# Performance work log

Measured on AMD Instinct MI355X. Metric: run time of the kernel, lower is better.

## Reference

```python
import jax, jax.numpy as jnp
import numpy as np

B, S, E = 2, 2048, 1024          # batch, seq, emb_size
H, D = 16, 64                     # heads, head_dim
NE, K = 8, 2                      # num_experts, top_k


def setup_inputs() -> dict:
    key = jax.random.key(0)
    ks = jax.random.split(key, 12)
    w = lambda k, shape: jax.random.normal(k, shape, jnp.float32) * 0.02
    return {
        "x": jax.random.normal(ks[0], (B, S, E), jnp.float32),
        "q_w": w(ks[1], (E, E)), "q_b": jnp.zeros((E,), jnp.float32),
        "k_w": w(ks[2], (E, E)), "k_b": jnp.zeros((E,), jnp.float32),
        "v_w": w(ks[3], (E, E)), "v_b": jnp.zeros((E,), jnp.float32),
        "gate_w": w(ks[4], (NE, E)), "gate_b": jnp.zeros((NE,), jnp.float32),
        "expert_w": w(ks[5], (NE, E, E)), "expert_b": jnp.zeros((NE, E), jnp.float32),
        "ffn_w": w(ks[6], (E, E)), "ffn_b": jnp.zeros((E,), jnp.float32),
    }


def _rope_cos_sin(seq_len, dim):
    inv_freq = 1.0 / (10000.0 ** (jnp.arange(0, dim, 2, dtype=jnp.float32) / dim))
    freqs = jnp.outer(jnp.arange(seq_len, dtype=jnp.float32), inv_freq)  # [S, D/2]
    emb = jnp.concatenate([freqs, freqs], axis=-1)                        # [S, D]
    return jnp.cos(emb), jnp.sin(emb)


def _rotate_half(x):
    x1, x2 = jnp.split(x, 2, axis=-1)
    return jnp.concatenate([-x2, x1], axis=-1)


def reference(x, q_w, q_b, k_w, k_b, v_w, v_b, gate_w, gate_b, expert_w, expert_b, ffn_w, ffn_b):
    b, s, _ = x.shape
    q = (x @ q_w.T + q_b).reshape(b, s, H, D)
    k = (x @ k_w.T + k_b).reshape(b, s, H, D)
    v = (x @ v_w.T + v_b).reshape(b, s, H, D)

    cos, sin = _rope_cos_sin(s, D)          # [S, D]
    cos = cos[None, :, None, :]
    sin = sin[None, :, None, :]
    q = q * cos + _rotate_half(q) * sin
    k = k * cos + _rotate_half(k) * sin

    # full (memory-efficient-style) attention, scale 1/sqrt(D)
    scores = jnp.einsum('bqhd,bkhd->bhqk', q, k) / jnp.sqrt(jnp.float32(D))
    attn = jax.nn.softmax(scores, axis=-1)
    attn_out = jnp.einsum('bhqk,bkhd->bqhd', attn, v).reshape(b, s, E)

    # MoE: dense-compute all experts, gather top-k, weighted combine
    gates = jax.nn.softmax(attn_out @ gate_w.T + gate_b, axis=-1)        # [B,S,NE]
    top_gates, top_idx = jax.lax.top_k(gates, K)                          # [B,S,K]
    # Linear per expert: y = x W^T + b,  expert_w: [NE, out, in]
    expert_outputs = jnp.einsum('bsi,noi->bsno', attn_out, expert_w) + expert_b  # [B,S,NE,E]
    sel = jnp.take_along_axis(expert_outputs, top_idx[..., None], axis=2)        # [B,S,K,E]
    moe_out = jnp.einsum('bsk,bskh->bsh', top_gates, sel)                        # [B,S,E]

    # dropout is identity at inference; ffn + residual
    return moe_out @ ffn_w.T + ffn_b + x
```

## Files before the change

### kernel.cpp

```cpp
#include <hip/hip_runtime.h>
#include <hip/hip_bf16.h>

#define B_ 2
#define S_ 2048
#define E_ 1024
#define H_ 16
#define D_ 64
#define NE_ 8
#define TOKENS (B_*S_)
#define QSCALE 0.18033688011112043f

typedef __attribute__((ext_vector_type(8))) short bf16x8;
typedef __attribute__((ext_vector_type(4))) float f32x4;
typedef __attribute__((ext_vector_type(16))) float f32x16;
typedef unsigned short u16;
typedef unsigned int u32;
typedef __attribute__((ext_vector_type(4))) u32 u32x4;

#if __has_builtin(__builtin_amdgcn_exp2f)
#define EXP2(x) __builtin_amdgcn_exp2f(x)
#else
#define EXP2(x) exp2f(x)
#endif

__device__ __forceinline__ u16 f2bf(float f) {
    u32 u = __float_as_uint(f);
    u32 r = u + 0x7fffu + ((u >> 16) & 1u);
    return (u16)(r >> 16);
}
__device__ __forceinline__ float bf2f(u16 h) {
    return __uint_as_float(((u32)h) << 16);
}
__device__ __forceinline__ void gl2lds16(const void* g, void* l) {
    __builtin_amdgcn_global_load_lds(
        (__attribute__((address_space(1))) void*)(g),
        (__attribute__((address_space(3))) void*)(l), 16, 0, 0);
}
#define MFMA16(a,b,c) __builtin_amdgcn_mfma_f32_16x16x32_bf16(a,b,c,0,0,0)
#define MFMA32(a,b,c) __builtin_amdgcn_mfma_f32_32x32x16_bf16(a,b,c,0,0,0)

__global__ void cvt_all_k(
    const float* __restrict__ x,  const float* __restrict__ qw,
    const float* __restrict__ kw, const float* __restrict__ vw,
    const float* __restrict__ fw, const float* __restrict__ ew,
    u16* __restrict__ xh,  u16* __restrict__ qwh, u16* __restrict__ kwh,
    u16* __restrict__ vwh, u16* __restrict__ fwh, u16* __restrict__ ewh,
    float2* __restrict__ tab)
{
    const int blk = blockIdx.x;
    if (blk >= 16384) {
        const int idx = (blk - 16384) * 256 + threadIdx.x;
        const int s = idx >> 5, d1 = idx & 31;
        const float inv = exp2f(-(float)d1 * 0.41524101186091903f);
        float sn, cs;
        sincosf((float)s * inv, &sn, &cs);
        tab[idx] = make_float2(cs, sn);
        return;
    }
    const float* s; u16* d; int off;
    if (blk < 4096)      { s = x;  d = xh;  off = blk; }
    else if (blk < 5120) { s = qw; d = qwh; off = blk - 4096; }
    else if (blk < 6144) { s = kw; d = kwh; off = blk - 5120; }
    else if (blk < 7168) { s = vw; d = vwh; off = blk - 6144; }
    else if (blk < 8192) { s = fw; d = fwh; off = blk - 7168; }
    else                 { s = ew; d = ewh; off = blk - 8192; }
    const size_t i = (size_t)off * 256 + threadIdx.x;
    const float4 v = *(const float4*)(s + i * 4);
    ushort4 H = {f2bf(v.x), f2bf(v.y), f2bf(v.z), f2bf(v.w)};
    *(ushort4*)(d + i * 4) = H;
}

__global__ __launch_bounds__(256,2) void gemm_qkv(
    const u16* __restrict__ Ah,
    const u16* __restrict__ qwh, const u16* __restrict__ kwh,
    const u16* __restrict__ vwh,
    const float* __restrict__ q_b, const float* __restrict__ k_b,
    const float* __restrict__ v_b,
    const float2* __restrict__ tab,
    u16* __restrict__ Qhb, u16* __restrict__ Khb, u16* __restrict__ Vtb)
{
    __shared__ __align__(16) u16 sA[128*32], sB[128*32];
    const int z = blockIdx.z;
    const u16* Bh = (z == 0) ? qwh : (z == 1) ? kwh : vwh;
    const float* bias = (z == 0) ? q_b : (z == 1) ? k_b : v_b;
    const int t = threadIdx.x;
    const int m0 = blockIdx.y * 128, n0 = blockIdx.x * 128;
    const int lane = t & 63, w = t >> 6;
    const int wm = w >> 1, wn = w & 1;
    const int lr = lane & 15, qd = lane >> 4;
    f32x4 acc[4][4] = {};
    const size_t gA = (size_t)(m0 + (t >> 2)) * E_ + (t & 3) * 8;
    const size_t gB = (size_t)(n0 + (t >> 2)) * E_ + (t & 3) * 8;
    for (int k0 = 0; k0 < E_; k0 += 32) {
        #pragma unroll
        for (int is = 0; is < 2; is++) {
            const int ldo = (is * 256 + (t & 192)) * 16;
            const size_t ro = (size_t)is * 64 * E_;
            gl2lds16(Ah + gA + ro + k0, (char*)sA + ldo);
            gl2lds16(Bh + gB + ro + k0, (char*)sB + ldo);
        }
        __syncthreads();
        bf16x8 af[4], bfr[4];
        #pragma unroll
        for (int i = 0; i < 4; i++) {
            af[i]  = *(const bf16x8*)&sA[(wm*64 + i*16 + lr)*32 + qd*8];
            bfr[i] = *(const bf16x8*)&sB[(wn*64 + i*16 + lr)*32 + qd*8];
        }
        #pragma unroll
        for (int i = 0; i < 4; i++)
            #pragma unroll
            for (int j = 0; j < 4; j++)
                acc[i][j] = MFMA16(af[i], bfr[j], acc[i][j]);
        __syncthreads();
    }
    const int head = (n0 + wn * 64) >> 6;
    if (z < 2) {
        u16* Oh = (z == 0) ? Qhb : Khb;
        const float osc = (z == 0) ? QSCALE : 1.0f;
        #pragma unroll
        for (int j = 0; j < 2; j++) {
            const int d1 = j * 16 + lr;
            const float b1 = bias[head * 64 + d1];
            const float b2 = bias[head * 64 + d1 + 32];
            #pragma unroll
            for (int i = 0; i < 4; i++) {
                #pragma unroll
                for (int r = 0; r < 4; r++) {
                    const int tok = m0 + wm*64 + i*16 + qd*4 + r;
                    const int bb = tok >> 11, ss = tok & (S_ - 1);
                    const float2 t2 = tab[ss * 32 + d1];
                    const float q1 = acc[i][j][r]   + b1;
                    const float q2 = acc[i][j+2][r] + b2;
                    const size_t o = (((size_t)bb * H_ + head) * S_ + ss) * 64 + d1;
                    Oh[o]    = f2bf((q1 * t2.x - q2 * t2.y) * osc);
                    Oh[o+32] = f2bf((q2 * t2.x + q1 * t2.y) * osc);
                }
            }
        }
    } else {
        #pragma unroll
        for (int j = 0; j < 4; j++) {
            const int d = j * 16 + lr;
            const float bv = bias[head * 64 + d];
            #pragma unroll
            for (int i = 0; i < 4; i++)
                #pragma unroll
                for (int r = 0; r < 4; r++) {
                    const int tok = m0 + wm*64 + i*16 + qd*4 + r;
                    const int bb = tok >> 11, ss = tok & (S_ - 1);
                    Vtb[(((size_t)bb * H_ + head) * 64 + d) * S_ + ss] = f2bf(acc[i][j][r] + bv);
                }
        }
    }
}

__global__ __launch_bounds__(256,4) void attn_kernel(
    const u16* __restrict__ Q, const u16* __restrict__ K,
    const u16* __restrict__ Vt,
    float* __restrict__ Opart, float* __restrict__ lpart)
{
    __shared__ __align__(16) u16 sK[2][64*64];
    __shared__ __align__(16) u16 sV[2][64*64];
    const int t = threadIdx.x, lane = t & 63, w = t >> 6;
    const int lq = lane & 31, hi = lane >> 5;
    const int lin = blockIdx.x + (blockIdx.y << 4) + (blockIdx.z << 8);
    const int wg  = ((lin & 7) << 7) + (lin >> 3);
    const int q0 = (wg & 15) << 7;
    const int h  = (wg >> 4) & 15;
    const int zc = wg >> 8;
    const int b = zc & 1, sc = zc >> 1;
    const size_t bhS = ((size_t)b * H_ + h) * S_;
    const size_t bhD = ((size_t)b * H_ + h) * 64;
    bf16x8 qf[4];
    #pragma unroll
    for (int ks = 0; ks < 4; ks++)
        qf[ks] = *(const bf16x8*)&Q[(bhS + q0 + w*32 + lq) * 64 + ks*16 + hi*8];
    bf16x8 vOnes;
    #pragma unroll
    for (int i = 0; i < 8; i++) vOnes[i] = (short)0x3F80;
    f32x16 O[2] = {};
    f32x16 Ol = {};

    const int f0 = w*2, f1 = w*2 + 1;
    const int kR0 = (f0>>2)*32 + lq, kC0 = (f0&3)*16 + hi*8;
    const int kR1 = (f1>>2)*32 + lq, kC1 = (f1&3)*16 + hi*8;
    auto stage = [&](int bp, int j0) {
        gl2lds16(&K [(bhS + j0 + kR0)*64 + kC0], (char*)sK[bp] + f0*1024);
        gl2lds16(&K [(bhS + j0 + kR1)*64 + kC1], (char*)sK[bp] + f1*1024);
        gl2lds16(&Vt[(bhD + kR0)*S_ + j0 + kC0], (char*)sV[bp] + f0*1024);
        gl2lds16(&Vt[(bhD + kR1)*S_ + j0 + kC1], (char*)sV[bp] + f1*1024);
    };

    const int jbeg = sc * 1024;
    stage(0, jbeg);
    for (int jt = 0; jt < 16; ++jt) {
        const int cur = jt & 1;
        asm volatile("s_waitcnt vmcnt(0) lgkmcnt(0)" ::: "memory");
        __builtin_amdgcn_sched_barrier(0);
        __builtin_amdgcn_s_barrier();
        __builtin_amdgcn_sched_barrier(0);
        if (jt + 1 < 16) stage(cur ^ 1, jbeg + (jt + 1) * 64);
        u32 pk[16];
        #pragma unroll
        for (int kb = 0; kb < 2; kb++) {
            f32x16 Sv = {};
            __builtin_amdgcn_s_setprio(1);
            #pragma unroll
            for (int ks = 0; ks < 4; ks++) {
                const bf16x8 kf = *(const bf16x8*)&sK[cur][(kb*4 + ks)*512 + lane*8];
                Sv = MFMA32(kf, qf[ks], Sv);
            }
            __builtin_amdgcn_s_setprio(0);
            #pragma unroll
            for (int j = 0; j < 8; j++) {
                const float e0 = EXP2(Sv[2*j]);
                const float e1 = EXP2(Sv[2*j+1]);
                pk[kb*8 + j] = __builtin_amdgcn_perm(__float_as_uint(e1),
                                                     __float_as_uint(e0), 0x07060302u);
            }
        }
        #pragma unroll
        for (int ks = 0; ks < 4; ks++) {
            const int base = (ks >> 1)*8 + (ks & 1)*4;
            u32 a0 = pk[base],     b0 = pk[base + 2];
            u32 a1 = pk[base + 1], b1 = pk[base + 3];
            asm("v_permlane32_swap_b32 %0, %1" : "+v"(a0), "+v"(b0));
            asm("v_permlane32_swap_b32 %0, %1" : "+v"(a1), "+v"(b1));
            u32x4 fv; fv.x = a0; fv.y = a1; fv.z = b0; fv.w = b1;
            const bf16x8 pa = __builtin_bit_cast(bf16x8, fv);
            const bf16x8 vf0 = *(const bf16x8*)&sV[cur][(0*4 + ks)*512 + lane*8];
            const bf16x8 vf1 = *(const bf16x8*)&sV[cur][(1*4 + ks)*512 + lane*8];
            __builtin_amdgcn_s_setprio(1);
            O[0] = MFMA32(pa, vf0, O[0]);
            O[1] = MFMA32(pa, vf1, O[1]);
            Ol   = MFMA32(pa, vOnes, Ol);
            __builtin_amdgcn_s_setprio(0);
        }
    }
    float* Op = Opart + (size_t)sc * TOKENS * E_;
    float* lp = lpart + (size_t)sc * TOKENS * H_;
    if (lq == 0) {
        #pragma unroll
        for (int r = 0; r < 16; r++) {
            const int qr = (r & 3) + 8*(r >> 2) + 4*hi;
            lp[(size_t)(b*S_ + q0 + w*32 + qr) * H_ + h] = Ol[r];
        }
    }
    #pragma unroll
    for (int cb = 0; cb < 2; cb++)
        #pragma unroll
        for (int r = 0; r < 16; r++) {
            const int qr = (r & 3) + 8*(r >> 2) + 4*hi;
            Op[(size_t)(b*S_ + q0 + w*32 + qr) * E_ + h*64 + cb*32 + lq] = O[cb][r];
        }
}

__global__ __launch_bounds__(256) void combine_gate(
    const float* __restrict__ Opart, const float* __restrict__ lpart,
    const float* __restrict__ gate_w, const float* __restrict__ gate_b,
    u16* __restrict__ attn_bf, float* __restrict__ gval, int* __restrict__ eidx)
{
    __shared__ float red[4][NE_];
    __shared__ float lg8[NE_];
    const int tok = blockIdx.x;
    const int t = threadIdx.x;
    const int d4 = t * 4;
    const int h = d4 >> 6;
    const float l = lpart[(size_t)tok*H_ + h] + lpart[(size_t)(TOKENS + tok)*H_ + h];
    const float inv = 1.f / l;
    const float4 o1 = *(const float4*)&Opart[(size_t)tok*E_ + d4];
    const float4 o2 = *(const float4*)&Opart[(size_t)(TOKENS + tok)*E_ + d4];
    float v[4] = {(o1.x+o2.x)*inv, (o1.y+o2.y)*inv, (o1.z+o2.z)*inv, (o1.w+o2.w)*inv};
    ushort4 H4 = {f2bf(v[0]), f2bf(v[1]), f2bf(v[2]), f2bf(v[3])};
    *(ushort4*)&attn_bf[(size_t)tok*E_ + d4] = H4;
    float pe[NE_];
    #pragma unroll
    for (int e = 0; e < NE_; e++) {
        const float4 g = *(const float4*)&gate_w[e*E_ + d4];
        pe[e] = v[0]*g.x + v[1]*g.y + v[2]*g.z + v[3]*g.w;
    }
    #pragma unroll
    for (int e = 0; e < NE_; e++) {
        #pragma unroll
        for (int off = 32; off >= 1; off >>= 1)
            pe[e] += __shfl_xor(pe[e], off, 64);
    }
    const int w = t >> 6;
    if ((t & 63) == 0) {
        #pragma unroll
        for (int e = 0; e < NE_; e++) red[w][e] = pe[e];
    }
    __syncthreads();
    if (t < NE_)
        lg8[t] = red[0][t] + red[1][t] + red[2][t] + red[3][t] + gate_b[t];
    __syncthreads();
    if (t == 0) {
        float lg[NE_];
        #pragma unroll
        for (int e = 0; e < NE_; e++) lg[e] = lg8[e];
        float m = lg[0];
        #pragma unroll
        for (int e = 1; e < NE_; e++) m = fmaxf(m, lg[e]);
        float ex[NE_], ssum = 0.f;
        #pragma unroll
        for (int e = 0; e < NE_; e++) { ex[e] = __expf(lg[e]-m); ssum += ex[e]; }
        const float invs = 1.f / ssum;
        int i0 = 0;
        #pragma unroll
        for (int e = 1; e < NE_; e++) if (lg[e] > lg[i0]) i0 = e;
        int i1 = (i0 == 0) ? 1 : 0;
        #pragma unroll
        for (int e = 0; e < NE_; e++) if (e != i0 && lg[e] > lg[i1]) i1 = e;
        eidx[tok*2]     = i0;
        gval[tok*2]     = ex[i0]*invs;
        eidx[tok*2 + 1] = i1;
        gval[tok*2 + 1] = ex[i1]*invs;
    }
}

__global__ __launch_bounds__(256) void build_lists_kernel(
    const int* __restrict__ eidx, int* __restrict__ list, int* __restrict__ counts)
{
    __shared__ int lcnt[NE_], lbase[NE_];
    const int t = threadIdx.x;
    if (t < NE_) lcnt[t] = 0;
    __syncthreads();
    const int ent = blockIdx.x * 512 + t * 2;
    const int e0 = eidx[ent], e1 = eidx[ent + 1];
    const int p0 = atomicAdd(&lcnt[e0], 1);
    const int p1 = atomicAdd(&lcnt[e1], 1);
    __syncthreads();
    if (t < NE_) lbase[t] = atomicAdd(&counts[t], lcnt[t]);
    __syncthreads();
    list[e0 * TOKENS + lbase[e0] + p0] = ent;
    list[e1 * TOKENS + lbase[e1] + p1] = ent + 1;
}

__global__ __launch_bounds__(256,2) void gemm_expert(
    const u16* __restrict__ Abf, const u16* __restrict__ ewh,
    const float* __restrict__ eb, const int* __restrict__ list,
    const int* __restrict__ counts, const float* __restrict__ gval,
    u16* __restrict__ sel)
{
    const int e = blockIdx.z;
    const int cnt = counts[e];
    const int m0 = blockIdx.y * 128;
    if (m0 >= cnt) return;
    __shared__ __align__(16) u16 sA[128*32], sB[128*32];
    __shared__ int sEnt[128];
    const int t = threadIdx.x;
    if (t < 128) sEnt[t] = (m0 + t < cnt) ? list[e * TOKENS + m0 + t] : -1;
    __syncthreads();
    const int n0 = blockIdx.x * 128;
    const int lane = t & 63, w = t >> 6;
    const int wm = w >> 1, wn = w & 1;
    const int lr = lane & 15, qd = lane >> 4;
    const int e0 = sEnt[t >> 2], e1 = sEnt[64 + (t >> 2)];
    const u16* ga0 = Abf + (size_t)(e0 < 0 ? 0 : (e0 >> 1)) * E_ + (t & 3) * 8;
    const u16* ga1 = Abf + (size_t)(e1 < 0 ? 0 : (e1 >> 1)) * E_ + (t & 3) * 8;
    const u16* gb0 = ewh + (size_t)e * E_ * E_ + (size_t)(n0 + (t >> 2)) * E_ + (t & 3) * 8;
    const u16* gb1 = gb0 + 64 * E_;
    f32x4 acc[4][4] = {};
    for (int k0 = 0; k0 < E_; k0 += 32) {
        {
            const int l0 = (t & 192) * 16;
            const int l1 = (256 + (t & 192)) * 16;
            gl2lds16(ga0 + k0, (char*)sA + l0);
            gl2lds16(ga1 + k0, (char*)sA + l1);
            gl2lds16(gb0 + k0, (char*)sB + l0);
            gl2lds16(gb1 + k0, (char*)sB + l1);
        }
        __syncthreads();
        bf16x8 af[4], bfr[4];
        #pragma unroll
        for (int i = 0; i < 4; i++) {
            af[i]  = *(const bf16x8*)&sA[(wm*64 + i*16 + lr)*32 + qd*8];
            bfr[i] = *(const bf16x8*)&sB[(wn*64 + i*16 + lr)*32 + qd*8];
        }
        #pragma unroll
        for (int i = 0; i < 4; i++)
            #pragma unroll
            for (int j = 0; j < 4; j++)
                acc[i][j] = MFMA16(af[i], bfr[j], acc[i][j]);
        __syncthreads();
    }
    #pragma unroll
    for (int i = 0; i < 4; i++)
        #pragma unroll
        for (int r = 0; r < 4; r++) {
            const int local = wm*64 + i*16 + qd*4 + r;
            const int ent = sEnt[local];
            if (ent < 0) continue;
            const float g = gval[ent];
            #pragma unroll
            for (int j = 0; j < 4; j++) {
                const int col = n0 + wn*64 + j*16 + lr;
                sel[(size_t)ent * E_ + col] = f2bf((acc[i][j][r] + eb[e * E_ + col]) * g);
            }
        }
}

__global__ void combine_kernel(const u16* __restrict__ sel, u16* __restrict__ moe)
{
    const int g = blockIdx.x * 256 + threadIdx.x;
    const int tok = g >> 8;
    const int c = (g & 255) * 4;
    const u16* a = sel + (size_t)tok * 2048 + c;
    float o[4];
    #pragma unroll
    for (int j = 0; j < 4; j++) o[j] = bf2f(a[j]) + bf2f(a[1024 + j]);
    ushort4 R = {f2bf(o[0]), f2bf(o[1]), f2bf(o[2]), f2bf(o[3])};
    *(ushort4*)(moe + (size_t)tok * E_ + c) = R;
}

__global__ __launch_bounds__(256,2) void gemm_ffn(
    const u16* __restrict__ Ah, const u16* __restrict__ Bh,
    const float* __restrict__ bias, const float* __restrict__ res,
    float* __restrict__ C)
{
    __shared__ __align__(16) u16 sA[128*32], sB[128*32];
    const int t = threadIdx.x;
    const int m0 = blockIdx.y * 128, n0 = blockIdx.x * 128;
    const int lane = t & 63, w = t >> 6;
    const int wm = w >> 1, wn = w & 1;
    const int lr = lane & 15, qd = lane >> 4;
    f32x4 acc[4][4] = {};
    const size_t gA = (size_t)(m0 + (t >> 2)) * E_ + (t & 3) * 8;
    const size_t gB = (size_t)(n0 + (t >> 2)) * E_ + (t & 3) * 8;
    for (int k0 = 0; k0 < E_; k0 += 32) {
        #pragma unroll
        for (int is = 0; is < 2; is++) {
            const int ldo = (is * 256 + (t & 192)) * 16;
            const size_t ro = (size_t)is * 64 * E_;
            gl2lds16(Ah + gA + ro + k0, (char*)sA + ldo);
            gl2lds16(Bh + gB + ro + k0, (char*)sB + ldo);
        }
        __syncthreads();
        bf16x8 af[4], bfr[4];
        #pragma unroll
        for (int i = 0; i < 4; i++) {
            af[i]  = *(const bf16x8*)&sA[(wm*64 + i*16 + lr)*32 + qd*8];
            bfr[i] = *(const bf16x8*)&sB[(wn*64 + i*16 + lr)*32 + qd*8];
        }
        #pragma unroll
        for (int i = 0; i < 4; i++)
            #pragma unroll
            for (int j = 0; j < 4; j++)
                acc[i][j] = MFMA16(af[i], bfr[j], acc[i][j]);
        __syncthreads();
    }
    #pragma unroll
    for (int i = 0; i < 4; i++)
        #pragma unroll
        for (int r = 0; r < 4; r++) {
            const int tok = m0 + wm*64 + i*16 + qd*4 + r;
            #pragma unroll
            for (int j = 0; j < 4; j++) {
                const int col = n0 + wn*64 + j*16 + lr;
                C[(size_t)tok * E_ + col] = acc[i][j][r] + bias[col] + res[(size_t)tok * E_ + col];
            }
        }
}

extern "C" void kernel_launch(void* const* d_in, const int* in_sizes, int n_in,
                              void* d_out, int out_size, void* d_ws, size_t ws_size,
                              hipStream_t stream) {
    const float* x      = (const float*)d_in[0];
    const float* q_w    = (const float*)d_in[1];
    const float* q_b    = (const float*)d_in[2];
    const float* k_w    = (const float*)d_in[3];
    const float* k_b    = (const float*)d_in[4];
    const float* v_w    = (const float*)d_in[5];
    const float* v_b    = (const float*)d_in[6];
    const float* gate_w = (const float*)d_in[7];
    const float* gate_b = (const float*)d_in[8];
    const float* ew     = (const float*)d_in[9];
    const float* eb     = (const float*)d_in[10];
    const float* ffn_w  = (const float*)d_in[11];
    const float* ffn_b  = (const float*)d_in[12];
    float* out = (float*)d_out;

    char* p = (char*)d_ws;
    auto alloc = [&](size_t bytes) { char* r = p; p += (bytes + 255) & ~(size_t)255; return r; };
    u16* xh   = (u16*)alloc((size_t)TOKENS*E_*2);
    u16* qwh  = (u16*)alloc((size_t)E_*E_*2);
    u16* kwh  = (u16*)alloc((size_t)E_*E_*2);
    u16* vwh  = (u16*)alloc((size_t)E_*E_*2);
    u16* fwh  = (u16*)alloc((size_t)E_*E_*2);
    u16* ewh  = (u16*)alloc((size_t)NE_*E_*E_*2);
    u16* Qhb  = (u16*)alloc((size_t)TOKENS*E_*2);
    u16* Khb  = (u16*)alloc((size_t)TOKENS*E_*2);
    u16* Vtb  = (u16*)alloc((size_t)TOKENS*E_*2);
    u16* abf  = (u16*)alloc((size_t)TOKENS*E_*2);
    float* Opart = (float*)alloc((size_t)2*TOKENS*E_*4);
    float* lpart = (float*)alloc((size_t)2*TOKENS*H_*4);
    u16* selb = (u16*)alloc((size_t)2*TOKENS*E_*2);
    u16* moeb = (u16*)alloc((size_t)TOKENS*E_*2);
    float2* rtab = (float2*)alloc((size_t)S_*32*8);
    float* gvl = (float*)alloc((size_t)2*TOKENS*4);
    int*   eix = (int*)alloc((size_t)2*TOKENS*4);
    int*   lst = (int*)alloc((size_t)NE_*TOKENS*4);
    int*   cnt = (int*)alloc(256);

    hipMemsetAsync(cnt, 0, 256, stream);

    cvt_all_k<<<16640, 256, 0, stream>>>(x, q_w, k_w, v_w, ffn_w, ew,
                                         xh, qwh, kwh, vwh, fwh, ewh, rtab);

    gemm_qkv<<<dim3(8,32,3), 256, 0, stream>>>(xh, qwh, kwh, vwh,
                                               q_b, k_b, v_b, rtab,
                                               Qhb, Khb, Vtb);

    attn_kernel<<<dim3(16,16,4), 256, 0, stream>>>(Qhb, Khb, Vtb, Opart, lpart);

    combine_gate<<<TOKENS, 256, 0, stream>>>(Opart, lpart, gate_w, gate_b,
                                             abf, gvl, eix);
    build_lists_kernel<<<TOKENS/256, 256, 0, stream>>>(eix, lst, cnt);
    gemm_expert<<<dim3(8,32,8), 256, 0, stream>>>(abf, ewh, eb, lst, cnt, gvl, selb);
    combine_kernel<<<4096, 256, 0, stream>>>(selb, moeb);
    gemm_ffn<<<dim3(8,32), 256, 0, stream>>>(moeb, fwh, ffn_b, x, out);
}
```

Baseline: 297.9 us.

## Load K/V fragments directly from global into registers, dropping LDS staging

The attention kernel no longer stages K and V tiles through double-buffered shared memory with barriers. Each wave now loads its own K and V MFMA fragments straight from global memory into registers, and the loop is unrolled by two so loads can overlap compute. This removes LDS traffic and the per-tile block barrier. In exchange, the four waves of a block each fetch the same K/V data redundantly, register pressure rises (launch bounds lowered to 3 blocks per SM), and load latency is hidden only by unrolling and occupancy.

```diff
diff --git a/kernel.cpp b/kernel.cpp
--- a/kernel.cpp
+++ b/kernel.cpp
@@ -154,13 +154,11 @@
     }
 }
 
-__global__ __launch_bounds__(256,4) void attn_kernel(
+__global__ __launch_bounds__(256,3) void attn_kernel(
     const u16* __restrict__ Q, const u16* __restrict__ K,
     const u16* __restrict__ Vt,
     float* __restrict__ Opart, float* __restrict__ lpart)
 {
-    __shared__ __align__(16) u16 sK[2][64*64];
-    __shared__ __align__(16) u16 sV[2][64*64];
     const int t = threadIdx.x, lane = t & 63, w = t >> 6;
     const int lq = lane & 31, hi = lane >> 5;
     const int lin = blockIdx.x + (blockIdx.y << 4) + (blockIdx.z << 8);
@@ -178,45 +176,54 @@
     bf16x8 vOnes;
     #pragma unroll
     for (int i = 0; i < 8; i++) vOnes[i] = (short)0x3F80;
-    f32x16 O[2] = {};
+    f32x16 O0 = {}, O1 = {};
     f32x16 Ol = {};
 
-    const int f0 = w*2, f1 = w*2 + 1;
-    const int kR0 = (f0>>2)*32 + lq, kC0 = (f0&3)*16 + hi*8;
-    const int kR1 = (f1>>2)*32 + lq, kC1 = (f1&3)*16 + hi*8;
-    auto stage = [&](int bp, int j0) {
-        gl2lds16(&K [(bhS + j0 + kR0)*64 + kC0], (char*)sK[bp] + f0*1024);
-        gl2lds16(&K [(bhS + j0 + kR1)*64 + kC1], (char*)sK[bp] + f1*1024);
-        gl2lds16(&Vt[(bhD + kR0)*S_ + j0 + kC0], (char*)sV[bp] + f0*1024);
-        gl2lds16(&Vt[(bhD + kR1)*S_ + j0 + kC1], (char*)sV[bp] + f1*1024);
-    };
-
+    const u16* Kb = K  + (bhS + lq) * 64 + hi * 8;
+    const u16* Vb = Vt + (bhD + lq) * S_ + hi * 8;
     const int jbeg = sc * 1024;
-    stage(0, jbeg);
+
+    #pragma unroll 2
     for (int jt = 0; jt < 16; ++jt) {
-        const int cur = jt & 1;
-        asm volatile("s_waitcnt vmcnt(0) lgkmcnt(0)" ::: "memory");
-        __builtin_amdgcn_sched_barrier(0);
-        __builtin_amdgcn_s_barrier();
-        __builtin_amdgcn_sched_barrier(0);
-        if (jt + 1 < 16) stage(cur ^ 1, jbeg + (jt + 1) * 64);
+        const int j0 = jbeg + jt * 64;
+        bf16x8 kr0[4], kr1[4], vr0[4], vr1[4];
+        #pragma unroll
+        for (int ks = 0; ks < 4; ks++) {
+            kr0[ks] = *(const bf16x8*)(Kb + (size_t)j0 * 64 + ks*16);
+            kr1[ks] = *(const bf16x8*)(Kb + (size_t)(j0 + 32) * 64 + ks*16);
+        }
+        #pragma unroll
+        for (int ks = 0; ks < 4; ks++) {
+            vr0[ks] = *(const bf16x8*)(Vb + j0 + ks*16);
+            vr1[ks] = *(const bf16x8*)(Vb + (size_t)32 * S_ + j0 + ks*16);
+        }
         u32 pk[16];
-        #pragma unroll
-        for (int kb = 0; kb < 2; kb++) {
+        {
             f32x16 Sv = {};
             __builtin_amdgcn_s_setprio(1);
             #pragma unroll
-            for (int ks = 0; ks < 4; ks++) {
-                const bf16x8 kf = *(const bf16x8*)&sK[cur][(kb*4 + ks)*512 + lane*8];
-                Sv = MFMA32(kf, qf[ks], Sv);
-            }
+            for (int ks = 0; ks < 4; ks++) Sv = MFMA32(kr0[ks], qf[ks], Sv);
             __builtin_amdgcn_s_setprio(0);
             #pragma unroll
             for (int j = 0; j < 8; j++) {
                 const float e0 = EXP2(Sv[2*j]);
                 const float e1 = EXP2(Sv[2*j+1]);
-                pk[kb*8 + j] = __builtin_amdgcn_perm(__float_as_uint(e1),
-                                                     __float_as_uint(e0), 0x07060302u);
+                pk[j] = __builtin_amdgcn_perm(__float_as_uint(e1),
+                                              __float_as_uint(e0), 0x07060302u);
+            }
+        }
+        {
+            f32x16 Sv = {};
+            __builtin_amdgcn_s_setprio(1);
+            #pragma unroll
+            for (int ks = 0; ks < 4; ks++) Sv = MFMA32(kr1[ks], qf[ks], Sv);
+            __builtin_amdgcn_s_setprio(0);
+            #pragma unroll
+            for (int j = 0; j < 8; j++) {
+                const float e0 = EXP2(Sv[2*j]);
+                const float e1 = EXP2(Sv[2*j+1]);
+                pk[8 + j] = __builtin_amdgcn_perm(__float_as_uint(e1),
+                                                  __float_as_uint(e0), 0x07060302u);
             }
         }
         #pragma unroll
@@ -228,12 +235,10 @@
             asm("v_permlane32_swap_b32 %0, %1" : "+v"(a1), "+v"(b1));
             u32x4 fv; fv.x = a0; fv.y = a1; fv.z = b0; fv.w = b1;
             const bf16x8 pa = __builtin_bit_cast(bf16x8, fv);
-            const bf16x8 vf0 = *(const bf16x8*)&sV[cur][(0*4 + ks)*512 + lane*8];
-            const bf16x8 vf1 = *(const bf16x8*)&sV[cur][(1*4 + ks)*512 + lane*8];
             __builtin_amdgcn_s_setprio(1);
-            O[0] = MFMA32(pa, vf0, O[0]);
-            O[1] = MFMA32(pa, vf1, O[1]);
-            Ol   = MFMA32(pa, vOnes, Ol);
+            O0 = MFMA32(pa, vr0[ks], O0);
+            O1 = MFMA32(pa, vr1[ks], O1);
+            Ol = MFMA32(pa, vOnes, Ol);
             __builtin_amdgcn_s_setprio(0);
         }
     }
@@ -247,12 +252,15 @@
         }
     }
     #pragma unroll
-    for (int cb = 0; cb < 2; cb++)
-        #pragma unroll
-        for (int r = 0; r < 16; r++) {
-            const int qr = (r & 3) + 8*(r >> 2) + 4*hi;
-            Op[(size_t)(b*S_ + q0 + w*32 + qr) * E_ + h*64 + cb*32 + lq] = O[cb][r];
-        }
+    for (int r = 0; r < 16; r++) {
+        const int qr = (r & 3) + 8*(r >> 2) + 4*hi;
+        Op[(size_t)(b*S_ + q0 + w*32 + qr) * E_ + h*64 + lq] = O0[r];
+    }
+    #pragma unroll
+    for (int r = 0; r < 16; r++) {
+        const int qr = (r & 3) + 8*(r >> 2) + 4*hi;
+        Op[(size_t)(b*S_ + q0 + w*32 + qr) * E_ + h*64 + 32 + lq] = O1[r];
+    }
 }
 
 __global__ __launch_bounds__(256) void combine_gate(
```

Result: slower. 366.0 us (+22.9%).
